# Kernel optimization log

Measured on AMD Instinct MI355X. Metric: run time of the kernel, lower is better.

The kernel has to match this reference:

```python
import jax, jax.numpy as jnp
import numpy as np

EMB = 1024
N_HEAD = 16
HEAD = 64
D_FF = 4 * EMB
LN_EPS = 1e-5


def layernorm(x, g, b):
    mu = jnp.mean(x, axis=-1, keepdims=True)
    var = jnp.mean(jnp.square(x - mu), axis=-1, keepdims=True)
    return (x - mu) * jax.lax.rsqrt(var + LN_EPS) * g + b


def setup_inputs() -> dict:
    key = jax.random.key(0)
    ks = jax.random.split(key, 12)
    s = 0.02
    x = jax.random.normal(ks[0], (4, 2048, EMB), dtype=jnp.float32)
    # per-head Q/K/V projections (no bias), stacked along head axis
    Wq = jax.random.normal(ks[1], (N_HEAD, EMB, HEAD), dtype=jnp.float32) * s
    Wk = jax.random.normal(ks[2], (N_HEAD, EMB, HEAD), dtype=jnp.float32) * s
    Wv = jax.random.normal(ks[3], (N_HEAD, EMB, HEAD), dtype=jnp.float32) * s
    Wo = jax.random.normal(ks[4], (EMB, EMB), dtype=jnp.float32) * s
    bo = jnp.zeros((EMB,), dtype=jnp.float32)
    ln1_g = jnp.ones((EMB,), dtype=jnp.float32)
    ln1_b = jnp.zeros((EMB,), dtype=jnp.float32)
    W1 = jax.random.normal(ks[5], (EMB, D_FF), dtype=jnp.float32) * s
    b1 = jnp.zeros((D_FF,), dtype=jnp.float32)
    W2 = jax.random.normal(ks[6], (D_FF, EMB), dtype=jnp.float32) * s
    b2 = jnp.zeros((EMB,), dtype=jnp.float32)
    ln2_g = jnp.ones((EMB,), dtype=jnp.float32)
    ln2_b = jnp.zeros((EMB,), dtype=jnp.float32)
    return dict(x=x, Wq=Wq, Wk=Wk, Wv=Wv, Wo=Wo, bo=bo, ln1_g=ln1_g,
                ln1_b=ln1_b, W1=W1, b1=b1, W2=W2, b2=b2, ln2_g=ln2_g,
                ln2_b=ln2_b)


def reference(x, Wq, Wk, Wv, Wo, bo, ln1_g, ln1_b, W1, b1, W2, b2, ln2_g, ln2_b):
    B, T, _ = x.shape
    # fused multi-head QKV (equivalent to the per-head Python loop + concat)
    q = jnp.einsum('btd,hdk->bhtk', x, Wq)
    k = jnp.einsum('btd,hdk->bhtk', x, Wk)
    v = jnp.einsum('btd,hdk->bhtk', x, Wv)
    scores = jnp.einsum('bhtk,bhsk->bhts', q, k) / jnp.sqrt(jnp.float32(HEAD))
    att = jax.nn.softmax(scores, axis=-1)
    heads = jnp.einsum('bhts,bhsk->bhtk', att, v)           # [B,H,T,head]
    cat = heads.transpose(0, 2, 1, 3).reshape(B, T, EMB)     # concat over heads
    mha = cat @ Wo + bo
    x = x + layernorm(mha, ln1_g, ln1_b)                     # residual of LN(sublayer)
    ff = jax.nn.gelu(x @ W1 + b1, approximate=False) @ W2 + b2
    x = x + layernorm(ff, ln2_g, ln2_b)
    return x
```

## Files before the change

### kernel.cpp

```cpp
#include <hip/hip_runtime.h>
#include <math.h>


using u16 = unsigned short;
typedef __bf16 bf16x8 __attribute__((ext_vector_type(8)));
typedef __bf16 bf16x4 __attribute__((ext_vector_type(4)));
typedef unsigned short u16x8 __attribute__((ext_vector_type(8)));
typedef unsigned short u16x4 __attribute__((ext_vector_type(4)));
typedef float f32x4 __attribute__((ext_vector_type(4)));

#if defined(__has_builtin)
#if __has_builtin(__builtin_amdgcn_exp2f)
#define EXP2F(x) __builtin_amdgcn_exp2f(x)
#endif
#endif
#ifndef EXP2F
#define EXP2F(x) __expf((x) * 0.69314718055994531f)
#endif

__device__ __forceinline__ float bf2f(u16 h) {
  return __uint_as_float(((unsigned int)h) << 16);
}
__device__ __forceinline__ u16 f2bf(float f) {
  unsigned int u = __float_as_uint(f);
  u += 0x7fffu + ((u >> 16) & 1u);
  return (u16)(u >> 16);
}

__device__ __forceinline__ void gload_lds16(const void* g, void* l) {
  __builtin_amdgcn_global_load_lds(
      (__attribute__((address_space(1))) void*)(g),
      (__attribute__((address_space(3))) void*)(l), 16, 0, 0);
}

__global__ __launch_bounds__(256) void detect_dtype(const u16* __restrict__ x,
                                                    int* __restrict__ flag) {
  __shared__ int cnt[256];
  int c = 0;
#pragma unroll
  for (int j = 0; j < 8; ++j) {
    float v = bf2f(x[threadIdx.x * 8 + j]);
    float a = fabsf(v);
    if (a >= 1e-4f && a <= 64.0f) ++c;
  }
  cnt[threadIdx.x] = c;
  __syncthreads();
  if (threadIdx.x == 0) {
    int t = 0;
    for (int i = 0; i < 256; ++i) t += cnt[i];
    flag[0] = (t < 1638) ? 1 : 0;
  }
}

__global__ __launch_bounds__(256) void cvt_copy(const void* __restrict__ in,
                                                u16* __restrict__ out,
                                                const int* __restrict__ flagp,
                                                long n) {
  long idx = ((long)blockIdx.x * 256 + threadIdx.x) * 4;
  if (idx >= n) return;
  if (*flagp) {
    float4 v = *(const float4*)((const float*)in + idx);
    out[idx] = f2bf(v.x); out[idx + 1] = f2bf(v.y);
    out[idx + 2] = f2bf(v.z); out[idx + 3] = f2bf(v.w);
  } else {
    *(u16x4*)(out + idx) = *(const u16x4*)((const u16*)in + idx);
  }
}

__global__ __launch_bounds__(256) void cvt_vecs(
    const void* s0, const void* s1, const void* s2, const void* s3,
    const void* s4, const void* s5, const void* s6, u16* __restrict__ dst,
    const int* __restrict__ flagp) {
  const int lens[7] = {1024, 1024, 1024, 4096, 1024, 1024, 1024};
  const int offs[7] = {0, 1024, 2048, 3072, 7168, 8192, 9216};
  const void* srcs[7] = {s0, s1, s2, s3, s4, s5, s6};
  int w = blockIdx.x;
  int f = *flagp;
  for (int i = threadIdx.x; i < lens[w]; i += 256)
    dst[offs[w] + i] = f ? f2bf(((const float*)srcs[w])[i])
                         : ((const u16*)srcs[w])[i];
}

__global__ __launch_bounds__(256) void transpose_cvt(
    const void* __restrict__ in, u16* __restrict__ out, int R, int C,
    long inBS, long outBS, const int* __restrict__ flagp) {
  __shared__ u16 tile[32][33];
  int f = *flagp;
  u16* ob = out + (long)blockIdx.z * outBS;
  int c = blockIdx.x * 32 + threadIdx.x;
  int r0 = blockIdx.y * 32;
  if (f) {
    const float* ib = (const float*)in + (long)blockIdx.z * inBS;
#pragma unroll
    for (int i = threadIdx.y; i < 32; i += 8)
      tile[i][threadIdx.x] = f2bf(ib[(long)(r0 + i) * C + c]);
  } else {
    const u16* ib = (const u16*)in + (long)blockIdx.z * inBS;
#pragma unroll
    for (int i = threadIdx.y; i < 32; i += 8)
      tile[i][threadIdx.x] = ib[(long)(r0 + i) * C + c];
  }
  __syncthreads();
  int r = r0 + threadIdx.x;
  int c0 = blockIdx.x * 32;
#pragma unroll
  for (int i = threadIdx.y; i < 32; i += 8)
    ob[(long)(c0 + i) * R + r] = tile[threadIdx.x][i];
}

__global__ __launch_bounds__(256) void kv_frag(const u16* __restrict__ qkv,
                                               u16* __restrict__ KF,
                                               u16* __restrict__ VF) {
  __shared__ u16 Kt[64][72];
  __shared__ u16 Vt[64][72];
  const int jblk = blockIdx.x, bh = blockIdx.y;
  const int b = bh >> 4, h = bh & 15;
  const int tid = threadIdx.x;
  const long j0 = jblk * 64;

  {
    int tt = tid >> 2, c0 = (tid & 3) * 16;
    const u16* src = qkv + (long)(b * 2048 + j0 + tt) * 3072 + h * 64 + c0;
    *(u16x8*)(&Kt[tt][c0]) = *(const u16x8*)(src + 1024);
    *(u16x8*)(&Kt[tt][c0 + 8]) = *(const u16x8*)(src + 1024 + 8);
    *(u16x8*)(&Vt[tt][c0]) = *(const u16x8*)(src + 2048);
    *(u16x8*)(&Vt[tt][c0 + 8]) = *(const u16x8*)(src + 2048 + 8);
  }
  __syncthreads();

  long obase = ((long)bh * 32 + jblk) * 8 * 512;
#pragma unroll
  for (int si = 0; si < 2; ++si) {
    int s = tid * 2 + si;
    int f = s >> 6, ln = s & 63;
    int kt = f >> 2, nt = f & 3;
    int lr = ln & 15, lq = ln >> 4;
    u16x8 ko, vo;
#pragma unroll
    for (int j = 0; j < 8; ++j) {
      ko[j] = Kt[nt * 16 + lr][kt * 32 + lq * 8 + j];
      vo[j] = Vt[kt * 32 + lq * 8 + j][nt * 16 + lr];
    }
    *(u16x8*)(KF + obase + (long)s * 8) = ko;
    *(u16x8*)(VF + obase + (long)s * 8) = vo;
  }
}

__device__ __forceinline__ bf16x8 fragld64(const u16* lb, int row, int ks,
                                           int lq) {
  int slot = ((ks << 2) | lq) ^ (row & 7);
  return *(const bf16x8*)(lb + row * 64 + slot * 8);
}

template <int EPI, int BN>
__global__ __launch_bounds__(512, 2) void gemm2ph(
    const u16* __restrict__ A, const u16* __restrict__ Bt,
    const u16* __restrict__ bias, u16* __restrict__ Cout,
    int M, int N, int K) {
  static_assert(BN == 256 || BN == 128, "");
  constexpr int NFQ = BN / 128;
  __shared__ u16 As[2][16384];
  __shared__ u16 Bs[2][BN * 64];
  const int tid = threadIdx.x;
  const int wave = tid >> 6, lane = tid & 63;
  const int lr = lane & 15, lq = lane >> 4;

  const int MT = M >> 8, NTt = N / BN;
  const int nwg = MT * NTt;
  int wg = blockIdx.x;
  if (!(nwg & 7)) wg = (wg & 7) * (nwg >> 3) + (wg >> 3);
  const int tm = wg % MT, tn = wg / MT;
  const long m0 = (long)tm << 8;
  const long n0 = (long)tn * BN;

  const int wm = (wave >> 2) << 7;
  const int wn = (wave & 3) * (BN / 4);

  const int srow = lane >> 3;
  const int skoff = ((lane & 7) ^ srow) * 8;

  auto stage = [&](int buf, int t) {
#pragma unroll
    for (int j = 0; j < 4; ++j)
      gload_lds16(
          A + (m0 + j * 64 + wave * 8 + srow) * (long)K + t * 64 + skoff,
          &As[buf][j * 4096 + (wave << 9)]);
#pragma unroll
    for (int j = 0; j < BN / 64; ++j)
      gload_lds16(
          Bt + (n0 + j * 64 + wave * 8 + srow) * (long)K + t * 64 + skoff,
          &Bs[buf][j * 4096 + (wave << 9)]);
  };

  f32x4 acc[8][2 * NFQ] = {};
  const int NT = K >> 6;
  int cur = 0;

  stage(0, 0);
  __syncthreads();

  for (int t = 0; t < NT; ++t) {
    const u16* Ab = As[cur];
    const u16* Bb = Bs[cur];
    if (t + 1 < NT) stage(cur ^ 1, t + 1);

    bf16x8 a_[4][2], b0_[NFQ][2], b1_[NFQ][2];
#pragma unroll
    for (int mf = 0; mf < 4; ++mf)
#pragma unroll
      for (int ks = 0; ks < 2; ++ks)
        a_[mf][ks] = fragld64(Ab, wm + mf * 16 + lr, ks, lq);
#pragma unroll
    for (int nf = 0; nf < NFQ; ++nf)
#pragma unroll
      for (int ks = 0; ks < 2; ++ks)
        b0_[nf][ks] = fragld64(Bb, wn + nf * 16 + lr, ks, lq);
#pragma unroll
    for (int mf = 0; mf < 4; ++mf)
#pragma unroll
      for (int nf = 0; nf < NFQ; ++nf)
#pragma unroll
        for (int ks = 0; ks < 2; ++ks)
          acc[mf][nf] = __builtin_amdgcn_mfma_f32_16x16x32_bf16(
              a_[mf][ks], b0_[nf][ks], acc[mf][nf], 0, 0, 0);
#pragma unroll
    for (int nf = 0; nf < NFQ; ++nf)
#pragma unroll
      for (int ks = 0; ks < 2; ++ks)
        b1_[nf][ks] = fragld64(Bb, wn + BN / 8 + nf * 16 + lr, ks, lq);
#pragma unroll
    for (int mf = 0; mf < 4; ++mf)
#pragma unroll
      for (int nf = 0; nf < NFQ; ++nf)
#pragma unroll
        for (int ks = 0; ks < 2; ++ks)
          acc[mf][NFQ + nf] = __builtin_amdgcn_mfma_f32_16x16x32_bf16(
              a_[mf][ks], b1_[nf][ks], acc[mf][NFQ + nf], 0, 0, 0);
#pragma unroll
    for (int mf = 0; mf < 4; ++mf)
#pragma unroll
      for (int ks = 0; ks < 2; ++ks)
        a_[mf][ks] = fragld64(Ab, wm + 64 + mf * 16 + lr, ks, lq);
#pragma unroll
    for (int mf = 0; mf < 4; ++mf)
#pragma unroll
      for (int nf = 0; nf < NFQ; ++nf)
#pragma unroll
        for (int ks = 0; ks < 2; ++ks)
          acc[4 + mf][NFQ + nf] = __builtin_amdgcn_mfma_f32_16x16x32_bf16(
              a_[mf][ks], b1_[nf][ks], acc[4 + mf][NFQ + nf], 0, 0, 0);
#pragma unroll
    for (int mf = 0; mf < 4; ++mf)
#pragma unroll
      for (int nf = 0; nf < NFQ; ++nf)
#pragma unroll
        for (int ks = 0; ks < 2; ++ks)
          acc[4 + mf][nf] = __builtin_amdgcn_mfma_f32_16x16x32_bf16(
              a_[mf][ks], b0_[nf][ks], acc[4 + mf][nf], 0, 0, 0);

    __syncthreads();
    cur ^= 1;
  }

  const int rq = lq * 4;
#pragma unroll
  for (int mf = 0; mf < 8; ++mf)
#pragma unroll
    for (int nf2 = 0; nf2 < 2 * NFQ; ++nf2) {
      const int col = (int)n0 + wn + nf2 * 16 + lr;
#pragma unroll
      for (int r = 0; r < 4; ++r) {
        const long row = m0 + wm + mf * 16 + rq + r;
        float v = acc[mf][nf2][r];
        if (EPI == 2) {
          v += bf2f(bias[col]);
          v = 0.5f * v * (1.0f + erff(v * 0.70710678118654752f));
        } else if (EPI == 3) {
          v += bf2f(bias[col]);
        }
        Cout[row * (long)N + col] = f2bf(v);
      }
    }
}

__global__ __launch_bounds__(256, 3) void flash_attn(
    const u16* __restrict__ qkv, const u16* __restrict__ KF,
    const u16* __restrict__ VF, u16* __restrict__ cat) {
  const int T = 2048, LD = 3072;
  const float QSCALE = 0.18033688011112042f;
  const float EXPC = 4.3280851226677321f;
  const int bh = blockIdx.y;
  const int b = bh >> 4, h = bh & 15;
  const int tid = threadIdx.x, wave = tid >> 6, lane = tid & 63;
  const int lr = lane & 15, lq = lane >> 4;

  __shared__ u16 Ps[4 * 32 * 64];
  u16* Pw = Ps + wave * 32 * 64;

  const u16* Qb = qkv + (long)(b * 2048) * LD + h * 64;
  const long fbase = (long)bh * 32 * 8 * 512;

  bf16x8 aq[2][2];
#pragma unroll
  for (int st = 0; st < 2; ++st) {
    int qrow = blockIdx.x * 128 + wave * 32 + st * 16 + lr;
#pragma unroll
    for (int kt = 0; kt < 2; ++kt) {
      u16x8 q = *(const u16x8*)(Qb + (long)qrow * LD + kt * 32 + lq * 8);
      bf16x8 t;
#pragma unroll
      for (int j = 0; j < 8; ++j) t[j] = (__bf16)(bf2f(q[j]) * QSCALE);
      aq[st][kt] = t;
    }
  }

  f32x4 o[2][4] = {};
  float lsum[2] = {0.0f, 0.0f};

  for (int jblk = 0; jblk < T / 64; ++jblk) {
    const u16* kf = KF + fbase + (long)jblk * 8 * 512;
    const u16* vf = VF + fbase + (long)jblk * 8 * 512;

    bf16x8 bk[2][4];
#pragma unroll
    for (int kt = 0; kt < 2; ++kt)
#pragma unroll
      for (int nt = 0; nt < 4; ++nt)
        bk[kt][nt] = *(const bf16x8*)(kf + (kt * 4 + nt) * 512 + lane * 8);

    f32x4 s[2][4] = {};
    __builtin_amdgcn_s_setprio(1);
#pragma unroll
    for (int st = 0; st < 2; ++st)
#pragma unroll
      for (int nt = 0; nt < 4; ++nt)
#pragma unroll
        for (int kt = 0; kt < 2; ++kt)
          s[st][nt] = __builtin_amdgcn_mfma_f32_16x16x32_bf16(
              bk[kt][nt], aq[st][kt], s[st][nt], 0, 0, 0);
    __builtin_amdgcn_s_setprio(0);

    bf16x8 bv[2][4];
#pragma unroll
    for (int kt = 0; kt < 2; ++kt)
#pragma unroll
      for (int nt = 0; nt < 4; ++nt)
        bv[kt][nt] = *(const bf16x8*)(vf + (kt * 4 + nt) * 512 + lane * 8);

#pragma unroll
    for (int st = 0; st < 2; ++st)
#pragma unroll
      for (int nt = 0; nt < 4; ++nt) {
        f32x4 p;
#pragma unroll
        for (int r = 0; r < 4; ++r) p[r] = EXP2F(s[st][nt][r] - EXPC);
        lsum[st] += (p[0] + p[1]) + (p[2] + p[3]);
        bf16x4 pk;
#pragma unroll
        for (int r = 0; r < 4; ++r) pk[r] = (__bf16)p[r];
        int wph = (nt * 2 + (lq >> 1)) ^ (lr & 7);
        *(bf16x4*)(Pw + (st * 16 + lr) * 64 + wph * 8 + (lq & 1) * 4) = pk;
      }

#pragma unroll
    for (int st = 0; st < 2; ++st)
#pragma unroll
      for (int kt = 0; kt < 2; ++kt) {
        bf16x8 ap = *(const bf16x8*)(
            Pw + (st * 16 + lr) * 64 + (((kt * 4 + lq) ^ (lr & 7)) * 8));
        __builtin_amdgcn_s_setprio(1);
#pragma unroll
        for (int nt = 0; nt < 4; ++nt)
          o[st][nt] = __builtin_amdgcn_mfma_f32_16x16x32_bf16(
              ap, bv[kt][nt], o[st][nt], 0, 0, 0);
        __builtin_amdgcn_s_setprio(0);
      }
  }

#pragma unroll
  for (int st = 0; st < 2; ++st) {
    lsum[st] += __shfl_xor(lsum[st], 16, 64);
    lsum[st] += __shfl_xor(lsum[st], 32, 64);
  }

  u16* ob = cat + (long)(b * 2048) * 1024 + h * 64;
#pragma unroll
  for (int st = 0; st < 2; ++st) {
    int trow = blockIdx.x * 128 + wave * 32 + st * 16 + lq * 4;
#pragma unroll
    for (int r = 0; r < 4; ++r) {
      float linv = 1.0f / __shfl(lsum[st], lq * 4 + r, 64);
#pragma unroll
      for (int nt = 0; nt < 4; ++nt)
        ob[(long)(trow + r) * 1024 + nt * 16 + lr] = f2bf(o[st][nt][r] * linv);
    }
  }
}

__global__ __launch_bounds__(256) void ln_residual(
    const u16* __restrict__ y, const void* __restrict__ res, int res_raw,
    const u16* __restrict__ g, const u16* __restrict__ bb,
    void* __restrict__ out, const int* __restrict__ flagp, int final_out) {
  const long row = blockIdx.x;
  const int tid = threadIdx.x, wave = tid >> 6, lane = tid & 63;
  u16x4 yv = *(const u16x4*)(y + row * 1024 + tid * 4);
  float yy[4];
#pragma unroll
  for (int j = 0; j < 4; ++j) yy[j] = bf2f(yv[j]);
  float s1 = yy[0] + yy[1] + yy[2] + yy[3];
  float s2 = yy[0] * yy[0] + yy[1] * yy[1] + yy[2] * yy[2] + yy[3] * yy[3];
#pragma unroll
  for (int off = 1; off < 64; off <<= 1) {
    s1 += __shfl_xor(s1, off, 64);
    s2 += __shfl_xor(s2, off, 64);
  }
  __shared__ float ws1[4], ws2[4];
  if (lane == 0) { ws1[wave] = s1; ws2[wave] = s2; }
  __syncthreads();
  float t1 = ws1[0] + ws1[1] + ws1[2] + ws1[3];
  float t2 = ws2[0] + ws2[1] + ws2[2] + ws2[3];
  float mu = t1 * (1.0f / 1024.0f);
  float var = t2 * (1.0f / 1024.0f) - mu * mu;
  float rstd = rsqrtf(var + 1e-5f);
  int i = tid * 4;
  bool f32in = res_raw && (*flagp);
  bool f32out = final_out && (*flagp);
#pragma unroll
  for (int j = 0; j < 4; ++j) {
    float rv = f32in ? ((const float*)res)[row * 1024 + i + j]
                     : bf2f(((const u16*)res)[row * 1024 + i + j]);
    float o = rv + (yy[j] - mu) * rstd * bf2f(g[i + j]) + bf2f(bb[i + j]);
    if (f32out)
      ((float*)out)[row * 1024 + i + j] = o;
    else
      ((u16*)out)[row * 1024 + i + j] = f2bf(o);
  }
}

extern "C" void kernel_launch(void* const* d_in, const int* in_sizes, int n_in,
                              void* d_out, int out_size, void* d_ws,
                              size_t ws_size, hipStream_t stream) {
  const void* x_raw = d_in[0];
  const void* Wq = d_in[1];
  const void* Wk = d_in[2];
  const void* Wv = d_in[3];
  const void* Wo = d_in[4];
  const void* bo = d_in[5];
  const void* ln1g = d_in[6];
  const void* ln1b = d_in[7];
  const void* W1 = d_in[8];
  const void* b1 = d_in[9];
  const void* W2 = d_in[10];
  const void* b2 = d_in[11];
  const void* ln2g = d_in[12];
  const void* ln2b = d_in[13];

  char* ws = (char*)d_ws;
  u16* qkv = (u16*)(ws + 0);
  u16* mha = (u16*)(ws + 0);
  u16* h1 = (u16*)(ws + 0);
  u16* cat = (u16*)(ws + 50331648);
  u16* KF = (u16*)(ws + 67108864);
  u16* ff = (u16*)(ws + 67108864);
  u16* xb = (u16*)(ws + 83886080);
  u16* VF = (u16*)(ws + 83886080);
  u16* x1 = (u16*)(ws + 83886080);
  u16* wqkvt = (u16*)(ws + 100663296);
  u16* wot = (u16*)(ws + 106954752);
  u16* w1t = (u16*)(ws + 109051904);
  u16* w2t = (u16*)(ws + 117440512);
  u16* vecs = (u16*)(ws + 125829120);
  int* flag = (int*)(ws + 125853696);

  const u16* v_bo = vecs + 0;
  const u16* v_l1g = vecs + 1024;
  const u16* v_l1b = vecs + 2048;
  const u16* v_b1 = vecs + 3072;
  const u16* v_b2 = vecs + 7168;
  const u16* v_l2g = vecs + 8192;
  const u16* v_l2b = vecs + 9216;

  detect_dtype<<<1, 256, 0, stream>>>((const u16*)x_raw, flag);
  cvt_copy<<<8192, 256, 0, stream>>>(x_raw, xb, flag, 8388608L);
  cvt_vecs<<<7, 256, 0, stream>>>(bo, ln1g, ln1b, b1, b2, ln2g, ln2b, vecs, flag);

  dim3 tb(32, 8);
  transpose_cvt<<<dim3(2, 32, 16), tb, 0, stream>>>(Wq, wqkvt, 1024, 64, 65536, 65536, flag);
  transpose_cvt<<<dim3(2, 32, 16), tb, 0, stream>>>(Wk, wqkvt + 1048576, 1024, 64, 65536, 65536, flag);
  transpose_cvt<<<dim3(2, 32, 16), tb, 0, stream>>>(Wv, wqkvt + 2097152, 1024, 64, 65536, 65536, flag);
  transpose_cvt<<<dim3(32, 32, 1), tb, 0, stream>>>(Wo, wot, 1024, 1024, 0, 0, flag);
  transpose_cvt<<<dim3(128, 32, 1), tb, 0, stream>>>(W1, w1t, 1024, 4096, 0, 0, flag);
  transpose_cvt<<<dim3(32, 128, 1), tb, 0, stream>>>(W2, w2t, 4096, 1024, 0, 0, flag);

  gemm2ph<0, 128><<<768, 512, 0, stream>>>(xb, wqkvt, nullptr, qkv, 8192, 3072, 1024);
  kv_frag<<<dim3(32, 64), 256, 0, stream>>>(qkv, KF, VF);
  flash_attn<<<dim3(16, 64), 256, 0, stream>>>(qkv, KF, VF, cat);
  gemm2ph<3, 128><<<256, 512, 0, stream>>>(cat, wot, v_bo, mha, 8192, 1024, 1024);
  ln_residual<<<8192, 256, 0, stream>>>(mha, x_raw, 1, v_l1g, v_l1b, x1, flag, 0);
  gemm2ph<2, 256><<<512, 512, 0, stream>>>(x1, w1t, v_b1, h1, 8192, 4096, 1024);
  gemm2ph<3, 128><<<256, 512, 0, stream>>>(h1, w2t, v_b2, ff, 8192, 1024, 4096);
  ln_residual<<<8192, 256, 0, stream>>>(ff, x1, 0, v_l2g, v_l2b, d_out, flag, 1);
}
```

Measured before the change: 621.9 us.

## Add triple-buffered LDS GEMM kernel for QKV, output and FFN2 projections

Adds a new GEMM kernel that keeps three LDS stages and prefetches tile t+2 while computing tile t. This lets global-to-LDS loads overlap two iterations of MFMA work with a single barrier per step. It also adds an 8-way workgroup swizzle for L2 locality. It replaces the two-phase GEMM for the N=128-tile launches (QKV, Wo, W2) but keeps the N=256 FFN1 path. The cost is more LDS (144KB per block), which limits occupancy.

```diff
diff --git a/kernel.cpp b/kernel.cpp
--- a/kernel.cpp
+++ b/kernel.cpp
@@ -267,6 +267,133 @@
   for (int mf = 0; mf < 8; ++mf)
 #pragma unroll
     for (int nf2 = 0; nf2 < 2 * NFQ; ++nf2) {
+      const int col = (int)n0 + wn + nf2 * 16 + lr;
+#pragma unroll
+      for (int r = 0; r < 4; ++r) {
+        const long row = m0 + wm + mf * 16 + rq + r;
+        float v = acc[mf][nf2][r];
+        if (EPI == 2) {
+          v += bf2f(bias[col]);
+          v = 0.5f * v * (1.0f + erff(v * 0.70710678118654752f));
+        } else if (EPI == 3) {
+          v += bf2f(bias[col]);
+        }
+        Cout[row * (long)N + col] = f2bf(v);
+      }
+    }
+}
+
+template <int EPI>
+__global__ __launch_bounds__(512, 2) void gemm3buf(
+    const u16* __restrict__ A, const u16* __restrict__ Bt,
+    const u16* __restrict__ bias, u16* __restrict__ Cout,
+    int M, int N, int K) {
+  __shared__ u16 As[3][16384];
+  __shared__ u16 Bs[3][8192];
+  const int tid = threadIdx.x;
+  const int wave = tid >> 6, lane = tid & 63;
+  const int lr = lane & 15, lq = lane >> 4;
+
+  const int MT = M >> 8, NTt = N >> 7;
+  const int nwg = MT * NTt;
+  int wg = blockIdx.x;
+  if (!(nwg & 7)) wg = (wg & 7) * (nwg >> 3) + (wg >> 3);
+  const int tm = wg % MT, tn = wg / MT;
+  const long m0 = (long)tm << 8;
+  const long n0 = (long)tn << 7;
+
+  const int wm = (wave >> 2) << 7;
+  const int wn = (wave & 3) * 32;
+
+  const int srow = lane >> 3;
+  const int skoff = ((lane & 7) ^ srow) * 8;
+
+  auto stage = [&](u16* ab, u16* bb, int t) {
+#pragma unroll
+    for (int j = 0; j < 4; ++j)
+      gload_lds16(
+          A + (m0 + j * 64 + wave * 8 + srow) * (long)K + t * 64 + skoff,
+          ab + j * 4096 + (wave << 9));
+#pragma unroll
+    for (int j = 0; j < 2; ++j)
+      gload_lds16(
+          Bt + (n0 + j * 64 + wave * 8 + srow) * (long)K + t * 64 + skoff,
+          bb + j * 4096 + (wave << 9));
+  };
+
+  u16 *pa0 = &As[0][0], *pa1 = &As[1][0], *pa2 = &As[2][0];
+  u16 *pb0 = &Bs[0][0], *pb1 = &Bs[1][0], *pb2 = &Bs[2][0];
+
+  f32x4 acc[8][2] = {};
+  const int NT = K >> 6;
+
+  stage(pa0, pb0, 0);
+  stage(pa1, pb1, 1);
+  asm volatile("s_waitcnt vmcnt(6)" ::: "memory");
+  __builtin_amdgcn_s_barrier();
+  __builtin_amdgcn_sched_barrier(0);
+
+  for (int t = 0; t < NT; ++t) {
+    const bool pf = (t + 2 < NT);
+    if (pf) stage(pa2, pb2, t + 2);
+
+    bf16x8 a_[4][2], b0_[2], b1_[2];
+#pragma unroll
+    for (int mf = 0; mf < 4; ++mf)
+#pragma unroll
+      for (int ks = 0; ks < 2; ++ks)
+        a_[mf][ks] = fragld64(pa0, wm + mf * 16 + lr, ks, lq);
+#pragma unroll
+    for (int ks = 0; ks < 2; ++ks) b0_[ks] = fragld64(pb0, wn + lr, ks, lq);
+#pragma unroll
+    for (int mf = 0; mf < 4; ++mf)
+#pragma unroll
+      for (int ks = 0; ks < 2; ++ks)
+        acc[mf][0] = __builtin_amdgcn_mfma_f32_16x16x32_bf16(
+            a_[mf][ks], b0_[ks], acc[mf][0], 0, 0, 0);
+#pragma unroll
+    for (int ks = 0; ks < 2; ++ks)
+      b1_[ks] = fragld64(pb0, wn + 16 + lr, ks, lq);
+#pragma unroll
+    for (int mf = 0; mf < 4; ++mf)
+#pragma unroll
+      for (int ks = 0; ks < 2; ++ks)
+        acc[mf][1] = __builtin_amdgcn_mfma_f32_16x16x32_bf16(
+            a_[mf][ks], b1_[ks], acc[mf][1], 0, 0, 0);
+#pragma unroll
+    for (int mf = 0; mf < 4; ++mf)
+#pragma unroll
+      for (int ks = 0; ks < 2; ++ks)
+        a_[mf][ks] = fragld64(pa0, wm + 64 + mf * 16 + lr, ks, lq);
+#pragma unroll
+    for (int mf = 0; mf < 4; ++mf)
+#pragma unroll
+      for (int ks = 0; ks < 2; ++ks)
+        acc[4 + mf][1] = __builtin_amdgcn_mfma_f32_16x16x32_bf16(
+            a_[mf][ks], b1_[ks], acc[4 + mf][1], 0, 0, 0);
+#pragma unroll
+    for (int mf = 0; mf < 4; ++mf)
+#pragma unroll
+      for (int ks = 0; ks < 2; ++ks)
+        acc[4 + mf][0] = __builtin_amdgcn_mfma_f32_16x16x32_bf16(
+            a_[mf][ks], b0_[ks], acc[4 + mf][0], 0, 0, 0);
+
+    if (pf)
+      asm volatile("s_waitcnt vmcnt(6) lgkmcnt(0)" ::: "memory");
+    else
+      asm volatile("s_waitcnt vmcnt(0) lgkmcnt(0)" ::: "memory");
+    __builtin_amdgcn_s_barrier();
+    __builtin_amdgcn_sched_barrier(0);
+
+    u16* ta = pa0; pa0 = pa1; pa1 = pa2; pa2 = ta;
+    u16* tb = pb0; pb0 = pb1; pb1 = pb2; pb2 = tb;
+  }
+
+  const int rq = lq * 4;
+#pragma unroll
+  for (int mf = 0; mf < 8; ++mf)
+#pragma unroll
+    for (int nf2 = 0; nf2 < 2; ++nf2) {
       const int col = (int)n0 + wn + nf2 * 16 + lr;
 #pragma unroll
       for (int r = 0; r < 4; ++r) {
@@ -492,12 +619,12 @@
   transpose_cvt<<<dim3(128, 32, 1), tb, 0, stream>>>(W1, w1t, 1024, 4096, 0, 0, flag);
   transpose_cvt<<<dim3(32, 128, 1), tb, 0, stream>>>(W2, w2t, 4096, 1024, 0, 0, flag);
 
-  gemm2ph<0, 128><<<768, 512, 0, stream>>>(xb, wqkvt, nullptr, qkv, 8192, 3072, 1024);
+  gemm3buf<0><<<768, 512, 0, stream>>>(xb, wqkvt, nullptr, qkv, 8192, 3072, 1024);
   kv_frag<<<dim3(32, 64), 256, 0, stream>>>(qkv, KF, VF);
   flash_attn<<<dim3(16, 64), 256, 0, stream>>>(qkv, KF, VF, cat);
-  gemm2ph<3, 128><<<256, 512, 0, stream>>>(cat, wot, v_bo, mha, 8192, 1024, 1024);
+  gemm3buf<3><<<256, 512, 0, stream>>>(cat, wot, v_bo, mha, 8192, 1024, 1024);
   ln_residual<<<8192, 256, 0, stream>>>(mha, x_raw, 1, v_l1g, v_l1b, x1, flag, 0);
   gemm2ph<2, 256><<<512, 512, 0, stream>>>(x1, w1t, v_b1, h1, 8192, 4096, 1024);
-  gemm2ph<3, 128><<<256, 512, 0, stream>>>(h1, w2t, v_b2, ff, 8192, 1024, 4096);
+  gemm3buf<3><<<256, 512, 0, stream>>>(h1, w2t, v_b2, ff, 8192, 1024, 4096);
   ln_residual<<<8192, 256, 0, stream>>>(ff, x1, 0, v_l2g, v_l2b, d_out, flag, 1);
 }
```

Result: no change. 624.2 us (+0.4%).
